# Kernel optimization log

Measured on AMD Instinct MI355X. Metric: run time of the kernel, lower is better.

## Reference

```python
import jax, jax.numpy as jnp
import numpy as np

B, C, H, W, NH = 16, 384, 28, 28, 6
S = H * W
EPS = 1e-5
SCALE = C ** -0.5  # note: original scales by dim**-0.5, not head_dim**-0.5


def setup_inputs():
    key = jax.random.key(0)
    ks = jax.random.split(key, 5)
    return {
        "x1": jax.random.normal(ks[0], (B, S, C), jnp.float32),
        "h1": H, "w1": W,
        "x2": jax.random.normal(ks[1], (B, S, C), jnp.float32),
        "h2": H, "w2": W,
        # stacked params for the 9 conv branches: q1,k1,v1,q2,k2,v2,q3,k3,v3
        "dw_w": jax.random.normal(ks[2], (9, C, 1, 3, 3), jnp.float32) * 0.1,
        "bn_gamma": jnp.ones((9, C), jnp.float32),
        "bn_beta": jnp.zeros((9, C), jnp.float32),
        "pw_w": jax.random.normal(ks[3], (9, C, C), jnp.float32) * (C ** -0.5),
        "pw_b": jnp.zeros((9, C), jnp.float32),
        "lin_w": jax.random.normal(ks[4], (9, C, C), jnp.float32) * (C ** -0.5),
    }


def _conv_branch(img, dw, g, b, pw, pwb):
    # depthwise 3x3 conv (no bias) -> train-mode BatchNorm2d -> 1x1 conv (bias)
    y = jax.lax.conv_general_dilated(
        img, dw, (1, 1), ((1, 1), (1, 1)),
        feature_group_count=img.shape[1],
        dimension_numbers=('NCHW', 'OIHW', 'NCHW'))
    mu = y.mean(axis=(0, 2, 3), keepdims=True)
    var = ((y - mu) ** 2).mean(axis=(0, 2, 3), keepdims=True)  # biased var, like torch BN
    y = (y - mu) * jax.lax.rsqrt(var + EPS) * g[None, :, None, None] + b[None, :, None, None]
    y = jnp.einsum('bchw,oc->bohw', y, pw) + pwb[None, :, None, None]
    return y.reshape(y.shape[0], y.shape[1], -1).transpose(0, 2, 1)  # b (h w) c


def _heads(x, w):
    # Linear (no bias): y = x @ w.T, then 'b t (h d) -> b h t d'
    y = jnp.einsum('btc,oc->bto', x, w)
    b, t, c = y.shape
    return y.reshape(b, t, NH, c // NH).transpose(0, 2, 1, 3)


def _attn(q, k, v):
    s = jnp.einsum('bhld,bhtd->bhlt', q, k) * SCALE
    a = jax.nn.softmax(s, axis=-1)
    o = jnp.einsum('bhlt,bhtd->bhld', a, v)
    b, h, t, d = o.shape
    # NOTE: original torch does .view(b, t, h*d) on a (b,h,t,d) tensor WITHOUT
    # transposing heads next to depth; replicate that raw reshape exactly.
    return o.reshape(b, t, h * d)


def _forward(x1, h1, w1, x2, h2, w2, dw_w, bn_gamma, bn_beta, pw_w, pw_b, lin_w):
    b, _, c = x1.shape
    i1 = x1.reshape(b, h1, w1, c).transpose(0, 3, 1, 2)  # b c h w
    i2 = x2.reshape(b, h2, w2, c).transpose(0, 3, 1, 2)
    i3 = i1 + i2
    imgs = (i1, i2, i3)
    outs = []
    for br in range(3):
        q = _conv_branch(imgs[br], dw_w[3*br+0], bn_gamma[3*br+0], bn_beta[3*br+0], pw_w[3*br+0], pw_b[3*br+0])
        k = _conv_branch(imgs[br], dw_w[3*br+1], bn_gamma[3*br+1], bn_beta[3*br+1], pw_w[3*br+1], pw_b[3*br+1])
        v = _conv_branch(imgs[br], dw_w[3*br+2], bn_gamma[3*br+2], bn_beta[3*br+2], pw_w[3*br+2], pw_b[3*br+2])
        # branch 3 reuses branch-2 Linear weights (bug in original source, replicated)
        li = 3 if br == 2 else 3 * br
        outs.append(_attn(_heads(q, lin_w[li+0]), _heads(k, lin_w[li+1]), _heads(v, lin_w[li+2])))
    return tuple(outs)


def reference(x1, h1, w1, x2, h2, w2, dw_w, bn_gamma, bn_beta, pw_w, pw_b, lin_w):
    return _forward(x1, h1, w1, x2, h2, w2, dw_w, bn_gamma, bn_beta, pw_w, pw_b, lin_w)
```

## Files before the change

### kernel.cpp

```cpp
#include <hip/hip_runtime.h>

typedef unsigned short u16;
typedef unsigned int u32;
typedef unsigned long long u64;

#define B_   16
#define C_   384
#define H_   28
#define W_   28
#define S_   784
#define NH_  6
#define HD_  64
#define BS_  (B_ * S_)
#define SCALE_ 0.05103103630798288f
#define EPS_ 1e-5f

typedef __attribute__((ext_vector_type(8))) short bf16x8;
typedef __attribute__((ext_vector_type(4))) float f32x4;

__device__ __forceinline__ float bf2f(u16 u) {
    return __uint_as_float(((u32)u) << 16);
}
__device__ __forceinline__ u16 f2bf(float f) {
    u32 x = __float_as_uint(f);
    u32 r = (x + 0x7fffu + ((x >> 16) & 1u)) >> 16;
    return (u16)r;
}

__device__ __forceinline__ void gld16(const u16* g, u16* l) {
    __builtin_amdgcn_global_load_lds(
        (__attribute__((address_space(1))) void*)g,
        (__attribute__((address_space(3))) void*)l, 16, 0, 0);
}

__launch_bounds__(384)
__global__ void k_conv(const float* __restrict__ x1, const float* __restrict__ x2,
                       const float* __restrict__ dw, u16* __restrict__ y,
                       float* __restrict__ part) {
    int c = threadIdx.x;
    int id = blockIdx.x;
    int xcd = id & 7;
    int j = id >> 3;
    int p = xcd + 8 * (j / 28);
    int h = j % 28;
    int g = p / 16;
    int b = p % 16;

    const float* pa = x1 + (size_t)b * S_ * C_ + c;
    const float* pb = x2 + (size_t)b * S_ * C_ + c;

    float wt[3][9];
#pragma unroll
    for (int i = 0; i < 3; ++i)
#pragma unroll
        for (int t = 0; t < 9; ++t)
            wt[i][t] = dw[((3 * g + i) * C_ + c) * 9 + t];

    float a[3][3];
#pragma unroll
    for (int dh = 0; dh < 3; ++dh) {
        int hh = h + dh - 1;
        bool hv = (hh >= 0) && (hh < H_);
        size_t o1 = (size_t)(hh * W_ + 0) * C_;
        size_t o2 = (size_t)(hh * W_ + 1) * C_;
        float v1 = 0.f, v2 = 0.f;
        if (hv) {
            if (g == 0)      { v1 = pa[o1];           v2 = pa[o2]; }
            else if (g == 1) { v1 = pb[o1];           v2 = pb[o2]; }
            else             { v1 = pa[o1] + pb[o1];  v2 = pa[o2] + pb[o2]; }
        }
        a[dh][0] = 0.f; a[dh][1] = v1; a[dh][2] = v2;
    }

    u16* dst[3];
#pragma unroll
    for (int i = 0; i < 3; ++i)
        dst[i] = y + ((size_t)((3 * g + i) * B_ + b) * S_ + h * W_) * C_ + c;

    float sum[3] = {0.f, 0.f, 0.f}, sq[3] = {0.f, 0.f, 0.f};

    for (int w = 0; w < W_; ++w) {
#pragma unroll
        for (int i = 0; i < 3; ++i) {
            const float* W9 = wt[i];
            float acc = a[0][0]*W9[0] + a[0][1]*W9[1] + a[0][2]*W9[2]
                      + a[1][0]*W9[3] + a[1][1]*W9[4] + a[1][2]*W9[5]
                      + a[2][0]*W9[6] + a[2][1]*W9[7] + a[2][2]*W9[8];
            sum[i] += acc;
            sq[i] = fmaf(acc, acc, sq[i]);
            dst[i][w * C_] = f2bf(acc);
        }
        int wn = w + 2;
        bool wv = (wn < W_);
#pragma unroll
        for (int dh = 0; dh < 3; ++dh) {
            a[dh][0] = a[dh][1];
            a[dh][1] = a[dh][2];
            int hh = h + dh - 1;
            float v = 0.f;
            if (wv && hh >= 0 && hh < H_) {
                size_t off = (size_t)(hh * W_ + wn) * C_;
                if (g == 0)      v = pa[off];
                else if (g == 1) v = pb[off];
                else             v = pa[off] + pb[off];
            }
            a[dh][2] = v;
        }
    }
#pragma unroll
    for (int i = 0; i < 3; ++i) {
        atomicAdd(&part[((3 * g + i) * C_ + c) * 2],     sum[i]);
        atomicAdd(&part[((3 * g + i) * C_ + c) * 2 + 1], sq[i]);
    }
}

__global__ void k_stats2(const float* __restrict__ part,
                         const float* __restrict__ gamma, const float* __restrict__ beta,
                         float* __restrict__ aScale, float* __restrict__ bShift) {
    int c = threadIdx.x;
    int idx = blockIdx.x;
    float s = part[(idx * C_ + c) * 2];
    float q = part[(idx * C_ + c) * 2 + 1];
    float mean = s / (float)BS_;
    float var  = q / (float)BS_ - mean * mean;
    float a = gamma[idx * C_ + c] * rsqrtf(var + EPS_);
    aScale[idx * C_ + c] = a;
    bShift[idx * C_ + c] = beta[idx * C_ + c] - mean * a;
}

__global__ void k_wcomb(const float* __restrict__ pw, const float* __restrict__ pwb,
                        const float* __restrict__ lin,
                        const float* __restrict__ aScale, const float* __restrict__ bShift,
                        u16* __restrict__ Wcb, float* __restrict__ Bc) {
    __shared__ float red[8];
    int og = blockIdx.x;
    int idx = blockIdx.y;
    int c = threadIdx.x;
    int wave = c >> 6, lane = c & 63;
    int li = (idx < 3) ? idx : 3 + (idx % 3);
    float acc[8];
#pragma unroll
    for (int k = 0; k < 8; ++k) acc[k] = 0.f;
    const float* pwm = pw + (idx * C_) * C_ + c;
    const float* lb  = lin + ((li * C_) + og * 8) * C_;
    for (int m = 0; m < C_; ++m) {
        float pv = pwm[m * C_];
#pragma unroll
        for (int k = 0; k < 8; ++k)
            acc[k] += lb[k * C_ + m] * pv;
    }
    float aS = aScale[idx * C_ + c];
    float bS = bShift[idx * C_ + c];
    float pwbc = pwb[idx * C_ + c];
    for (int k = 0; k < 8; ++k) {
        int o = og * 8 + k;
        Wcb[(idx * C_ + o) * C_ + c] = f2bf(acc[k] * aS);
        float v = acc[k] * bS + lin[(li * C_ + o) * C_ + c] * pwbc;
#pragma unroll
        for (int msk = 1; msk < 64; msk <<= 1) v += __shfl_xor(v, msk);
        if (lane == 0) red[wave] = v;
        __syncthreads();
        if (c == 0)
            Bc[idx * C_ + o] = red[0] + red[1] + red[2] + red[3] + red[4] + red[5];
        __syncthreads();
    }
}

__launch_bounds__(256)
__global__ void k_gemm(const u16* __restrict__ y, const u16* __restrict__ Wcb,
                       const float* __restrict__ Bc, u16* __restrict__ qkv) {
    __shared__ __align__(16) u16 ldsA[2][4096];
    __shared__ __align__(16) u16 ldsB[2][4096];

    int id = blockIdx.x;
    int xcd = id & 7;
    int kb = id >> 3;
    int zz = kb / 21;
    int t  = kb % 21;
    int z  = zz * 8 + xcd;
    int by = t / 7, bx = t % 7;
    int idx = z >> 4, b = z & 15;

    int tid = threadIdx.x;
    int wave = tid >> 6;
    int lane = tid & 63;
    int lq = lane & 15;
    int quad = lane >> 4;
    int o_base = by * 128 + (wave & 1) * 64;
    int s_base_w = bx * 128 + (wave >> 1) * 64;

    const u16* ybase = y + (size_t)(idx * B_ + b) * S_ * C_;
    const u16* wbase = Wcb + (size_t)idx * C_ * C_;

    int r0 = tid >> 2;
    int qs = (tid & 3) ^ ((r0 ^ (r0 >> 2)) & 3);
    int srA0 = bx * 128 + r0;       if (srA0 > S_ - 1) srA0 = S_ - 1;
    int srA1 = bx * 128 + r0 + 64;  if (srA1 > S_ - 1) srA1 = S_ - 1;
    const u16* gA0 = ybase + (size_t)srA0 * C_ + qs * 8;
    const u16* gA1 = ybase + (size_t)srA1 * C_ + qs * 8;
    const u16* gB0 = wbase + (size_t)(by * 128 + r0) * C_ + qs * 8;
    const u16* gB1 = wbase + (size_t)(by * 128 + r0 + 64) * C_ + qs * 8;
    int lo0 = wave * 512;
    int lo1 = 2048 + wave * 512;

#define STAGE(stg, kk) do {                          \
        gld16(gA0 + (kk) * 32, &ldsA[stg][lo0]);     \
        gld16(gA1 + (kk) * 32, &ldsA[stg][lo1]);     \
        gld16(gB0 + (kk) * 32, &ldsB[stg][lo0]);     \
        gld16(gB1 + (kk) * 32, &ldsB[stg][lo1]);     \
    } while (0)

    f32x4 acc[4][4];
#pragma unroll
    for (int i = 0; i < 4; ++i)
#pragma unroll
        for (int j = 0; j < 4; ++j) acc[i][j] = (f32x4){0.f,0.f,0.f,0.f};

    STAGE(0, 0);
    __syncthreads();

    int qoff = (quad ^ ((lq ^ (lq >> 2)) & 3)) * 8;
    bf16x8 af[4], bw[4];
#pragma unroll
    for (int ks = 0; ks < 12; ++ks) {
        int cur = ks & 1;
        if (ks < 11) STAGE(cur ^ 1, ks + 1);
#pragma unroll
        for (int mt = 0; mt < 4; ++mt) {
            int sl = (wave >> 1) * 64 + mt * 16 + lq;
            __builtin_memcpy(&af[mt], &ldsA[cur][sl * 32 + qoff], 16);
        }
#pragma unroll
        for (int nt = 0; nt < 4; ++nt) {
            int ol = (wave & 1) * 64 + nt * 16 + lq;
            __builtin_memcpy(&bw[nt], &ldsB[cur][ol * 32 + qoff], 16);
        }
#pragma unroll
        for (int mt = 0; mt < 4; ++mt)
#pragma unroll
            for (int nt = 0; nt < 4; ++nt)
                acc[mt][nt] = __builtin_amdgcn_mfma_f32_16x16x32_bf16(
                    af[mt], bw[nt], acc[mt][nt], 0, 0, 0);
        __syncthreads();
    }
#undef STAGE

    float bias[4];
#pragma unroll
    for (int nt = 0; nt < 4; ++nt) bias[nt] = Bc[idx * C_ + o_base + nt * 16 + lq];
    u16* obase = qkv + ((size_t)(idx * B_ + b) * S_) * C_;
#pragma unroll
    for (int mt = 0; mt < 4; ++mt) {
#pragma unroll
        for (int r = 0; r < 4; ++r) {
            int s = s_base_w + mt * 16 + quad * 4 + r;
            if (s >= S_) continue;
            u16* row = obase + (size_t)s * C_ + o_base + lq;
#pragma unroll
            for (int nt = 0; nt < 4; ++nt)
                row[nt * 16] = f2bf(acc[mt][nt][r] + bias[nt]);
        }
    }
}

__launch_bounds__(256)
__global__ void k_attn(const u16* __restrict__ qkv, float* __restrict__ out) {
    __shared__ __align__(16) u16 sm[13568];

    int id = blockIdx.x;
    int g8 = id & 7;
    int rest = id >> 3;
    int qtile = rest % 7;
    int zh = (rest / 7) * 8 + g8;
    int z = zh / 6, h = zh % 6;
    int br = z >> 4;
    int tid = threadIdx.x;
    int wave = tid >> 6;
    int lane = tid & 63;
    int lq = lane & 15;
    int quad = lane >> 4;

    int idxq = 3 * br;
    const u16* qp = qkv + (size_t)((idxq * B_ + (z & 15)) * S_) * C_ + h * HD_;
    const u16* kp = qkv + (size_t)(((idxq + 1) * B_ + (z & 15)) * S_) * C_ + h * HD_;
    const u16* vp = qkv + (size_t)(((idxq + 2) * B_ + (z & 15)) * S_) * C_ + h * HD_;

    int qbase = qtile * 128 + wave * 32;
    int qrA = qbase + lq;      if (qrA > S_ - 1) qrA = S_ - 1;
    int qrB = qbase + 16 + lq; if (qrB > S_ - 1) qrB = S_ - 1;
    const u16* qpa = qp + (size_t)qrA * C_ + quad * 8;
    const u16* qpb = qp + (size_t)qrB * C_ + quad * 8;
    bf16x8 aqA0 = *(const bf16x8*)qpa;
    bf16x8 aqA1 = *(const bf16x8*)(qpa + 32);
    bf16x8 aqB0 = *(const bf16x8*)qpb;
    bf16x8 aqB1 = *(const bf16x8*)(qpb + 32);

    f32x4 oA[4], oB[4];
#pragma unroll
    for (int i = 0; i < 4; ++i) { oA[i] = (f32x4){0.f,0.f,0.f,0.f}; oB[i] = oA[i]; }
    float rsA[4] = {0.f,0.f,0.f,0.f}, rsB[4] = {0.f,0.f,0.f,0.f};

    int t2 = (tid & 31) * 2;
    int dg = (tid >> 5) * 8;
    int baseA = 4352 + wave * 2304;
    int baseB = baseA + 16 * 72;

    for (int ch = 0; ch < 13; ++ch) {
        int tc = ch * 64;
        int tg0 = tc + t2;     if (tg0 > S_ - 1) tg0 = S_ - 1;
        int tg1 = tc + t2 + 1; if (tg1 > S_ - 1) tg1 = S_ - 1;
        bf16x8 v0 = *(const bf16x8*)(vp + (size_t)tg0 * C_ + dg);
        bf16x8 v1 = *(const bf16x8*)(vp + (size_t)tg1 * C_ + dg);
        __syncthreads();
#pragma unroll
        for (int e = 0; e < 8; ++e) {
            u32 pk = (u32)(u16)v0[e] | ((u32)(u16)v1[e] << 16);
            *(u32*)&sm[(dg + e) * 68 + t2] = pk;
        }
        __syncthreads();

#pragma unroll
        for (int tt = 0; tt < 4; ++tt) {
            bool live = (tc + tt * 16) < S_;
            int tg = tc + tt * 16 + lq; if (tg > S_ - 1) tg = S_ - 1;
            const u16* kptr = kp + (size_t)tg * C_ + quad * 8;
            bf16x8 bk0 = *(const bf16x8*)kptr;
            bf16x8 bk1 = *(const bf16x8*)(kptr + 32);
            f32x4 sA = {0.f,0.f,0.f,0.f}, sB = sA;
            sA = __builtin_amdgcn_mfma_f32_16x16x32_bf16(aqA0, bk0, sA, 0, 0, 0);
            sA = __builtin_amdgcn_mfma_f32_16x16x32_bf16(aqA1, bk1, sA, 0, 0, 0);
            sB = __builtin_amdgcn_mfma_f32_16x16x32_bf16(aqB0, bk0, sB, 0, 0, 0);
            sB = __builtin_amdgcn_mfma_f32_16x16x32_bf16(aqB1, bk1, sB, 0, 0, 0);
#pragma unroll
            for (int r = 0; r < 4; ++r) {
                float pa = live ? __expf(sA[r] * SCALE_) : 0.f;
                float pb = live ? __expf(sB[r] * SCALE_) : 0.f;
                u16 pba = (u16)(__float_as_uint(pa) >> 16);
                u16 pbb = (u16)(__float_as_uint(pb) >> 16);
                sm[baseA + (quad * 4 + r) * 72 + tt * 16 + lq] = pba;
                sm[baseB + (quad * 4 + r) * 72 + tt * 16 + lq] = pbb;
                rsA[r] += __uint_as_float((u32)pba << 16);
                rsB[r] += __uint_as_float((u32)pbb << 16);
            }
        }

        bf16x8 apA[2], apB[2];
#pragma unroll
        for (int n = 0; n < 2; ++n) {
            __builtin_memcpy(&apA[n], &sm[baseA + lq * 72 + n * 32 + quad * 8], 16);
            __builtin_memcpy(&apB[n], &sm[baseB + lq * 72 + n * 32 + quad * 8], 16);
        }
        const char* bp = (const char*)sm;
#pragma unroll
        for (int dt = 0; dt < 4; ++dt) {
#pragma unroll
            for (int kh = 0; kh < 2; ++kh) {
                union { u64 q[2]; bf16x8 v; } bv;
                int j = (dt * 16 + lq) * 68 + kh * 32 + quad * 8;
                bv.q[0] = *(const u64*)(bp + 2 * j);
                bv.q[1] = *(const u64*)(bp + 2 * (j + 4));
                oA[dt] = __builtin_amdgcn_mfma_f32_16x16x32_bf16(apA[kh], bv.v, oA[dt], 0, 0, 0);
                oB[dt] = __builtin_amdgcn_mfma_f32_16x16x32_bf16(apB[kh], bv.v, oB[dt], 0, 0, 0);
            }
        }
    }

#pragma unroll
    for (int msk = 1; msk <= 8; msk <<= 1)
#pragma unroll
        for (int r = 0; r < 4; ++r) {
            rsA[r] += __shfl_xor(rsA[r], msk);
            rsB[r] += __shfl_xor(rsB[r], msk);
        }

    size_t obase = ((size_t)z * NH_ + h) * S_ * HD_;
#pragma unroll
    for (int r = 0; r < 4; ++r) {
        int qa = qbase + quad * 4 + r;
        if (qa < S_) {
            float inv = 1.f / rsA[r];
            float* dst = out + obase + (size_t)qa * HD_ + lq;
            dst[0]  = oA[0][r] * inv;
            dst[16] = oA[1][r] * inv;
            dst[32] = oA[2][r] * inv;
            dst[48] = oA[3][r] * inv;
        }
        int qb = qbase + 16 + quad * 4 + r;
        if (qb < S_) {
            float inv = 1.f / rsB[r];
            float* dst = out + obase + (size_t)qb * HD_ + lq;
            dst[0]  = oB[0][r] * inv;
            dst[16] = oB[1][r] * inv;
            dst[32] = oB[2][r] * inv;
            dst[48] = oB[3][r] * inv;
        }
    }
}

extern "C" void kernel_launch(void* const* d_in, const int* in_sizes, int n_in,
                              void* d_out, int out_size, void* d_ws, size_t ws_size,
                              hipStream_t stream) {
    (void)in_sizes; (void)n_in; (void)out_size; (void)ws_size;
    const float* x1    = (const float*)d_in[0];
    const float* x2    = (const float*)d_in[3];
    const float* dw    = (const float*)d_in[6];
    const float* gamma = (const float*)d_in[7];
    const float* beta  = (const float*)d_in[8];
    const float* pw    = (const float*)d_in[9];
    const float* pwb   = (const float*)d_in[10];
    const float* lin   = (const float*)d_in[11];
    float* out = (float*)d_out;

    char* ws = (char*)d_ws;
    u16*  y   = (u16*)(ws + 28901376);
    u16*  qkv = (u16*)(ws + 115605504);
    u16*  Wcb = (u16*)(ws + 202309632);
    float* Bc = (float*)(ws + 204963840);
    float* aS = (float*)(ws + 204977664);
    float* bS = (float*)(ws + 204991488);
    float* part = (float*)(ws + 205005312);

    hipMemsetAsync(part, 0, 9 * C_ * 2 * sizeof(float), stream);
    k_conv  <<<dim3(1344), 384, 0, stream>>>(x1, x2, dw, y, part);
    k_stats2<<<dim3(9), 384, 0, stream>>>(part, gamma, beta, aS, bS);
    k_wcomb <<<dim3(48, 9), 384, 0, stream>>>(pw, pwb, lin, aS, bS, Wcb, Bc);
    k_gemm  <<<dim3(3024), 256, 0, stream>>>(y, Wcb, Bc, qkv);
    k_attn  <<<dim3(2016), 256, 0, stream>>>(qkv, out);
}
```

Measured before the change: 448.9 us.

## Restructure attention inner loop: swizzled V layout, packed P, exp2, peeled tail

Reworks the attention kernel's shared-memory plan. V is stored with an XOR swizzle so the PV operand loads become single 16-byte reads. The A and B probability tiles are packed into one u32 buffer, written with a perm instruction and unpacked on read, which cuts shared memory use. Softmax uses raw v_exp_f32 with a prescaled log2 factor. The last partial 64-token chunk is peeled out so the main loop drops its clamps and liveness checks. Launch bounds now request 6 blocks per SIMD, which may raise occupancy but risks register spills.

After: 674.4 us. +50.2%, slower.

```diff
diff --git a/kernel.cpp b/kernel.cpp
--- a/kernel.cpp
+++ b/kernel.cpp
@@ -13,6 +13,7 @@
 #define HD_  64
 #define BS_  (B_ * S_)
 #define SCALE_ 0.05103103630798288f
+#define LSC_   0.07362225484151387f
 #define EPS_ 1e-5f
 
 typedef __attribute__((ext_vector_type(8))) short bf16x8;
@@ -31,6 +32,12 @@
     __builtin_amdgcn_global_load_lds(
         (__attribute__((address_space(1))) void*)g,
         (__attribute__((address_space(3))) void*)l, 16, 0, 0);
+}
+
+__device__ __forceinline__ float exp2_fast(float x) {
+    float r;
+    asm("v_exp_f32 %0, %1" : "=v"(r) : "v"(x));
+    return r;
 }
 
 __launch_bounds__(384)
@@ -263,9 +270,9 @@
     }
 }
 
-__launch_bounds__(256)
+__launch_bounds__(256, 6)
 __global__ void k_attn(const u16* __restrict__ qkv, float* __restrict__ out) {
-    __shared__ __align__(16) u16 sm[13568];
+    __shared__ __align__(16) u16 sm[12544];
 
     int id = blockIdx.x;
     int g8 = id & 7;
@@ -302,28 +309,34 @@
 
     int t2 = (tid & 31) * 2;
     int dg = (tid >> 5) * 8;
-    int baseA = 4352 + wave * 2304;
-    int baseB = baseA + 16 * 72;
-
-    for (int ch = 0; ch < 13; ++ch) {
+    char* smb = (char*)sm;
+    u32* pb0 = (u32*)sm + 2048 + wave * 1056;
+    u32* pwr = pb0 + (quad * 4) * 66 + lq;
+    const u32* prd = pb0 + lq * 66 + quad * 8;
+    int sw = lq & 7;
+    int vrb0 = lq * 128 + ((quad ^ sw) << 4);
+    int vrb1 = lq * 128 + (((4 + quad) ^ sw) << 4);
+
+#define VSTAGE(TG0, TG1) do {                                              \
+        bf16x8 v0 = *(const bf16x8*)(vp + (size_t)(TG0) * C_ + dg);        \
+        bf16x8 v1 = *(const bf16x8*)(vp + (size_t)(TG1) * C_ + dg);        \
+        __syncthreads();                                                   \
+        _Pragma("unroll")                                                  \
+        for (int e = 0; e < 8; ++e) {                                      \
+            u32 pk = (u32)(u16)v0[e] | ((u32)(u16)v1[e] << 16);            \
+            *(u32*)(smb + (dg + e) * 128 + ((((t2 >> 3) ^ e)) << 4)        \
+                    + ((t2 & 7) << 1)) = pk;                               \
+        }                                                                  \
+        __syncthreads();                                                   \
+    } while (0)
+
+    for (int ch = 0; ch < 12; ++ch) {
         int tc = ch * 64;
-        int tg0 = tc + t2;     if (tg0 > S_ - 1) tg0 = S_ - 1;
-        int tg1 = tc + t2 + 1; if (tg1 > S_ - 1) tg1 = S_ - 1;
-        bf16x8 v0 = *(const bf16x8*)(vp + (size_t)tg0 * C_ + dg);
-        bf16x8 v1 = *(const bf16x8*)(vp + (size_t)tg1 * C_ + dg);
-        __syncthreads();
-#pragma unroll
-        for (int e = 0; e < 8; ++e) {
-            u32 pk = (u32)(u16)v0[e] | ((u32)(u16)v1[e] << 16);
-            *(u32*)&sm[(dg + e) * 68 + t2] = pk;
-        }
-        __syncthreads();
+        VSTAGE(tc + t2, tc + t2 + 1);
 
 #pragma unroll
         for (int tt = 0; tt < 4; ++tt) {
-            bool live = (tc + tt * 16) < S_;
-            int tg = tc + tt * 16 + lq; if (tg > S_ - 1) tg = S_ - 1;
-            const u16* kptr = kp + (size_t)tg * C_ + quad * 8;
+            const u16* kptr = kp + (size_t)(tc + tt * 16 + lq) * C_ + quad * 8;
             bf16x8 bk0 = *(const bf16x8*)kptr;
             bf16x8 bk1 = *(const bf16x8*)(kptr + 32);
             f32x4 sA = {0.f,0.f,0.f,0.f}, sB = sA;
@@ -333,37 +346,91 @@
             sB = __builtin_amdgcn_mfma_f32_16x16x32_bf16(aqB1, bk1, sB, 0, 0, 0);
 #pragma unroll
             for (int r = 0; r < 4; ++r) {
-                float pa = live ? __expf(sA[r] * SCALE_) : 0.f;
-                float pb = live ? __expf(sB[r] * SCALE_) : 0.f;
-                u16 pba = (u16)(__float_as_uint(pa) >> 16);
-                u16 pbb = (u16)(__float_as_uint(pb) >> 16);
-                sm[baseA + (quad * 4 + r) * 72 + tt * 16 + lq] = pba;
-                sm[baseB + (quad * 4 + r) * 72 + tt * 16 + lq] = pbb;
-                rsA[r] += __uint_as_float((u32)pba << 16);
-                rsB[r] += __uint_as_float((u32)pbb << 16);
+                float ea = exp2_fast(sA[r] * LSC_);
+                float eb = exp2_fast(sB[r] * LSC_);
+                u32 ua = __float_as_uint(ea) & 0xFFFF0000u;
+                u32 ub = __float_as_uint(eb) & 0xFFFF0000u;
+                rsA[r] += __uint_as_float(ua);
+                rsB[r] += __uint_as_float(ub);
+                pwr[r * 66 + tt * 16] = __builtin_amdgcn_perm(
+                    __float_as_uint(eb), __float_as_uint(ea), 0x07060302u);
             }
         }
 
         bf16x8 apA[2], apB[2];
 #pragma unroll
         for (int n = 0; n < 2; ++n) {
-            __builtin_memcpy(&apA[n], &sm[baseA + lq * 72 + n * 32 + quad * 8], 16);
-            __builtin_memcpy(&apB[n], &sm[baseB + lq * 72 + n * 32 + quad * 8], 16);
-        }
-        const char* bp = (const char*)sm;
+            u32 uu[8];
+            __builtin_memcpy(uu, prd + n * 32, 32);
+            union { u32 w[4]; bf16x8 v; } ca, cb;
+#pragma unroll
+            for (int jj = 0; jj < 4; ++jj) {
+                ca.w[jj] = __builtin_amdgcn_perm(uu[2*jj+1], uu[2*jj], 0x05040100u);
+                cb.w[jj] = __builtin_amdgcn_perm(uu[2*jj+1], uu[2*jj], 0x07060302u);
+            }
+            apA[n] = ca.v; apB[n] = cb.v;
+        }
+
 #pragma unroll
         for (int dt = 0; dt < 4; ++dt) {
-#pragma unroll
-            for (int kh = 0; kh < 2; ++kh) {
-                union { u64 q[2]; bf16x8 v; } bv;
-                int j = (dt * 16 + lq) * 68 + kh * 32 + quad * 8;
-                bv.q[0] = *(const u64*)(bp + 2 * j);
-                bv.q[1] = *(const u64*)(bp + 2 * (j + 4));
-                oA[dt] = __builtin_amdgcn_mfma_f32_16x16x32_bf16(apA[kh], bv.v, oA[dt], 0, 0, 0);
-                oB[dt] = __builtin_amdgcn_mfma_f32_16x16x32_bf16(apB[kh], bv.v, oB[dt], 0, 0, 0);
+            bf16x8 bv0, bv1;
+            __builtin_memcpy(&bv0, smb + dt * 2048 + vrb0, 16);
+            __builtin_memcpy(&bv1, smb + dt * 2048 + vrb1, 16);
+            oA[dt] = __builtin_amdgcn_mfma_f32_16x16x32_bf16(apA[0], bv0, oA[dt], 0, 0, 0);
+            oB[dt] = __builtin_amdgcn_mfma_f32_16x16x32_bf16(apB[0], bv0, oB[dt], 0, 0, 0);
+            oA[dt] = __builtin_amdgcn_mfma_f32_16x16x32_bf16(apA[1], bv1, oA[dt], 0, 0, 0);
+            oB[dt] = __builtin_amdgcn_mfma_f32_16x16x32_bf16(apB[1], bv1, oB[dt], 0, 0, 0);
+        }
+    }
+
+    {
+        int tc = 768;
+        int tg0 = tc + t2;     if (tg0 > S_ - 1) tg0 = S_ - 1;
+        int tg1 = tc + t2 + 1; if (tg1 > S_ - 1) tg1 = S_ - 1;
+        VSTAGE(tg0, tg1);
+
+        const u16* kptr = kp + (size_t)(tc + lq) * C_ + quad * 8;
+        bf16x8 bk0 = *(const bf16x8*)kptr;
+        bf16x8 bk1 = *(const bf16x8*)(kptr + 32);
+        f32x4 sA = {0.f,0.f,0.f,0.f}, sB = sA;
+        sA = __builtin_amdgcn_mfma_f32_16x16x32_bf16(aqA0, bk0, sA, 0, 0, 0);
+        sA = __builtin_amdgcn_mfma_f32_16x16x32_bf16(aqA1, bk1, sA, 0, 0, 0);
+        sB = __builtin_amdgcn_mfma_f32_16x16x32_bf16(aqB0, bk0, sB, 0, 0, 0);
+        sB = __builtin_amdgcn_mfma_f32_16x16x32_bf16(aqB1, bk1, sB, 0, 0, 0);
+#pragma unroll
+        for (int r = 0; r < 4; ++r) {
+            float ea = exp2_fast(sA[r] * LSC_);
+            float eb = exp2_fast(sB[r] * LSC_);
+            u32 ua = __float_as_uint(ea) & 0xFFFF0000u;
+            u32 ub = __float_as_uint(eb) & 0xFFFF0000u;
+            rsA[r] += __uint_as_float(ua);
+            rsB[r] += __uint_as_float(ub);
+            pwr[r * 66]      = __builtin_amdgcn_perm(
+                __float_as_uint(eb), __float_as_uint(ea), 0x07060302u);
+            pwr[r * 66 + 16] = 0;
+        }
+
+        bf16x8 apA0, apB0;
+        {
+            u32 uu[8];
+            __builtin_memcpy(uu, prd, 32);
+            union { u32 w[4]; bf16x8 v; } ca, cb;
+#pragma unroll
+            for (int jj = 0; jj < 4; ++jj) {
+                ca.w[jj] = __builtin_amdgcn_perm(uu[2*jj+1], uu[2*jj], 0x05040100u);
+                cb.w[jj] = __builtin_amdgcn_perm(uu[2*jj+1], uu[2*jj], 0x07060302u);
             }
-        }
-    }
+            apA0 = ca.v; apB0 = cb.v;
+        }
+#pragma unroll
+        for (int dt = 0; dt < 4; ++dt) {
+            bf16x8 bv0;
+            __builtin_memcpy(&bv0, smb + dt * 2048 + vrb0, 16);
+            oA[dt] = __builtin_amdgcn_mfma_f32_16x16x32_bf16(apA0, bv0, oA[dt], 0, 0, 0);
+            oB[dt] = __builtin_amdgcn_mfma_f32_16x16x32_bf16(apB0, bv0, oB[dt], 0, 0, 0);
+        }
+    }
+#undef VSTAGE
 
 #pragma unroll
     for (int msk = 1; msk <= 8; msk <<= 1)
```
